# Performance work log

Measured on AMD Instinct MI355X. Metric: run time of the kernel, lower is better.

## Reference

```python
import jax, jax.numpy as jnp
import numpy as np

N, E, F_IN, H, D, HID, G = 50000, 800000, 64, 4, 32, 128, 1024
NEG_SLOPE = 0.2


def setup_inputs():
    key = jax.random.key(0)
    ks = jax.random.split(key, 32)
    inp = {
        "x": jax.random.normal(ks[0], (N, F_IN), dtype=jnp.float32),
        "edge_index": jax.random.randint(ks[1], (2, E), 0, N, dtype=jnp.int64),
        "batch": jnp.sort(jax.random.randint(ks[2], (N,), 0, G, dtype=jnp.int64)),
    }
    dims = [F_IN, HID, HID]
    i = 3
    for l, din in enumerate(dims):
        s = 1.0 / np.sqrt(din)
        inp[f"Wl{l}"] = jax.random.normal(ks[i], (din, H * D), dtype=jnp.float32) * s; i += 1
        inp[f"bl{l}"] = jnp.zeros((H * D,), dtype=jnp.float32)
        inp[f"Wr{l}"] = jax.random.normal(ks[i], (din, H * D), dtype=jnp.float32) * s; i += 1
        inp[f"br{l}"] = jnp.zeros((H * D,), dtype=jnp.float32)
        inp[f"att{l}"] = jax.random.normal(ks[i], (H, D), dtype=jnp.float32) * (1.0 / np.sqrt(D)); i += 1
        inp[f"b{l}"] = jnp.zeros((H * D,), dtype=jnp.float32)
    inp["Wh"] = jax.random.normal(ks[i], (HID, 1), dtype=jnp.float32) * (1.0 / np.sqrt(HID))
    inp["bh"] = jnp.zeros((1,), dtype=jnp.float32)
    return inp


def gatv2_layer(x, src, dst, Wl, bl, Wr, br, att, b):
    # GATv2Conv (eval mode, no dropout): e_ij = att . leaky_relu(Wl x_j + Wr x_i)
    xl = (x @ Wl + bl).reshape(-1, H, D)   # source transform
    xr = (x @ Wr + br).reshape(-1, H, D)   # target transform
    m = xl[src] + xr[dst]                  # [E,H,D]
    e = jnp.where(m >= 0, m, NEG_SLOPE * m)
    score = jnp.einsum("ehd,hd->eh", e, att)          # [E,H]
    smax = jax.ops.segment_max(score, dst, num_segments=N)  # [N,H]
    expv = jnp.exp(score - smax[dst])
    denom = jax.ops.segment_sum(expv, dst, num_segments=N)
    alpha = expv / denom[dst]                          # softmax over in-edges of dst
    agg = jax.ops.segment_sum(alpha[:, :, None] * xl[src], dst, num_segments=N)
    return agg.reshape(-1, H * D) + b


def reference(x, edge_index, batch, Wl0, bl0, Wr0, br0, att0, b0,
              Wl1, bl1, Wr1, br1, att1, b1,
              Wl2, bl2, Wr2, br2, att2, b2, Wh, bh):
    src, dst = edge_index[0], edge_index[1]
    params = [(Wl0, bl0, Wr0, br0, att0, b0),
              (Wl1, bl1, Wr1, br1, att1, b1),
              (Wl2, bl2, Wr2, br2, att2, b2)]
    h = x
    for p in params:
        h = gatv2_layer(h, src, dst, *p)
        h = jax.nn.elu(h)  # dropout inactive in eval
    # global mean pool over graphs
    sums = jax.ops.segment_sum(h, batch, num_segments=G)
    cnt = jax.ops.segment_sum(jnp.ones((h.shape[0],), h.dtype), batch, num_segments=G)
    pooled = sums / jnp.maximum(cnt, 1.0)[:, None]
    return pooled @ Wh + bh
```

## Files before the change

### kernel.cpp

```cpp
#include <hip/hip_runtime.h>
#include <math.h>

#define N_NODES 50000
#define N_EDGES 800000
#define HD 128
#define GG 1024
#define NEG_SLOPE 0.2f
#define SCAN_B 1024
#define NB ((N_NODES + SCAN_B - 1) / SCAN_B)
#define LOG2E 1.4426950408889634f

#if __has_builtin(__builtin_amdgcn_exp2f)
#define EXP2F(x) __builtin_amdgcn_exp2f(x)
#else
#define EXP2F(x) exp2f(x)
#endif

typedef __attribute__((ext_vector_type(8))) short bf16x8;
typedef __attribute__((ext_vector_type(4))) float f32x4;

__device__ __forceinline__ unsigned short f2bf(float v) {
    unsigned u = __float_as_uint(v);
    u += 0x7fff + ((u >> 16) & 1);
    return (unsigned short)(u >> 16);
}
__device__ __forceinline__ float bf2f(unsigned short s) {
    return __uint_as_float((unsigned)s << 16);
}

__global__ void convert_x(const float* __restrict__ x, unsigned short* __restrict__ Xh,
                          unsigned short* __restrict__ Xl, int total)
{
    int i = blockIdx.x * 256 + threadIdx.x;
    if (i >= total) return;
    float v = x[i];
    unsigned short hi = f2bf(v);
    unsigned short lo = f2bf(v - bf2f(hi));
    Xh[i] = hi; Xl[i] = lo;
}

__global__ void convert_w_all(const float* __restrict__ W0l, const float* __restrict__ W0r,
                              const float* __restrict__ W1l, const float* __restrict__ W1r,
                              const float* __restrict__ W2l, const float* __restrict__ W2r,
                              unsigned short* __restrict__ Wth, unsigned short* __restrict__ Wtl)
{
    const int t = blockIdx.x * 256 + threadIdx.x;
    const float* Wl; const float* Wr;
    int c, k, o;
    if (t < 16384) {
        c = t >> 6; k = t & 63; o = t;
        Wl = W0l; Wr = W0r;
    } else if (t < 49152) {
        const int b = t - 16384; c = b >> 7; k = b & 127; o = 32768 + b;
        Wl = W1l; Wr = W1r;
    } else if (t < 81920) {
        const int b = t - 49152; c = b >> 7; k = b & 127; o = 65536 + b;
        Wl = W2l; Wr = W2r;
    } else return;
    const float v = (c < 128) ? Wl[(size_t)k * 128 + c] : Wr[(size_t)k * 128 + (c - 128)];
    const unsigned short hi = f2bf(v);
    Wth[o] = hi;
    Wtl[o] = f2bf(v - bf2f(hi));
}

template<int K>
__launch_bounds__(256)
__global__ void gemm_reg(const unsigned short* __restrict__ Xh, const unsigned short* __restrict__ Xl,
                         const unsigned short* __restrict__ Wth, const unsigned short* __restrict__ Wtl,
                         const float* __restrict__ bl, const float* __restrict__ br,
                         float* __restrict__ Cl, float* __restrict__ Cr, int n)
{
    constexpr int NCH = K / 32;
    constexpr int RT  = (N_NODES + 63) / 64;
    const int tid  = threadIdx.x;
    const int wave = tid >> 6;
    const int lane = tid & 63;
    const int quad = lane >> 4;
    const int l15  = lane & 15;
    const int wid  = blockIdx.x * 4 + wave;
    const int colid = wid & 7;
    const int cb32  = colid * 32;
    const int rs    = wid >> 3;
    const int NS    = (gridDim.x * 4) >> 3;

    bf16x8 Bh[NCH][2], Bo[NCH][2];
    #pragma unroll
    for (int ch = 0; ch < NCH; ch++)
        #pragma unroll
        for (int nt = 0; nt < 2; nt++) {
            const size_t wo = (size_t)(cb32 + nt * 16 + l15) * K + ch * 32 + quad * 8;
            Bh[ch][nt] = *(const bf16x8*)(Wth + wo);
            Bo[ch][nt] = *(const bf16x8*)(Wtl + wo);
        }

    const int cb = cb32 & 127;
    const float* bias = (colid < 4) ? bl : br;
    float* C = (colid < 4) ? Cl : Cr;
    float bv[2];
    bv[0] = bias[cb + l15];
    bv[1] = bias[cb + 16 + l15];

    for (int rt = rs; rt < RT; rt += NS) {
        const int row0 = rt * 64;
        f32x4 acc[4][2];
        #pragma unroll
        for (int mt = 0; mt < 4; mt++) {
            acc[mt][0] = (f32x4){0.f, 0.f, 0.f, 0.f};
            acc[mt][1] = (f32x4){0.f, 0.f, 0.f, 0.f};
        }
        #pragma unroll
        for (int ch = 0; ch < NCH; ch++) {
            bf16x8 ah[4], al[4];
            #pragma unroll
            for (int mt = 0; mt < 4; mt++) {
                int r = row0 + mt * 16 + l15;
                r = (r < n) ? r : (n - 1);
                const size_t go = (size_t)r * K + ch * 32 + quad * 8;
                ah[mt] = *(const bf16x8*)(Xh + go);
                al[mt] = *(const bf16x8*)(Xl + go);
            }
            #pragma unroll
            for (int nt = 0; nt < 2; nt++)
                #pragma unroll
                for (int mt = 0; mt < 4; mt++) {
                    acc[mt][nt] = __builtin_amdgcn_mfma_f32_16x16x32_bf16(ah[mt], Bh[ch][nt], acc[mt][nt], 0, 0, 0);
                    acc[mt][nt] = __builtin_amdgcn_mfma_f32_16x16x32_bf16(ah[mt], Bo[ch][nt], acc[mt][nt], 0, 0, 0);
                    acc[mt][nt] = __builtin_amdgcn_mfma_f32_16x16x32_bf16(al[mt], Bh[ch][nt], acc[mt][nt], 0, 0, 0);
                }
        }
        #pragma unroll
        for (int nt = 0; nt < 2; nt++)
            #pragma unroll
            for (int mt = 0; mt < 4; mt++)
                #pragma unroll
                for (int r = 0; r < 4; r++) {
                    const int row = row0 + mt * 16 + quad * 4 + r;
                    if (row < n)
                        C[(size_t)row * 128 + cb + nt * 16 + l15] = acc[mt][nt][r] + bv[nt];
                }
    }
}

__global__ void deg_hist(const int* __restrict__ dst, int* __restrict__ deg) {
    int e = blockIdx.x * 256 + threadIdx.x;
    if (e < N_EDGES) atomicAdd(&deg[dst[e]], 1);
}

__launch_bounds__(SCAN_B)
__global__ void scan_block(const int* __restrict__ deg, int* __restrict__ rowptr,
                           int* __restrict__ btot)
{
    __shared__ int s[SCAN_B];
    const int tid = threadIdx.x;
    const int i = blockIdx.x * SCAN_B + tid;
    int v = (i < N_NODES) ? deg[i] : 0;
    s[tid] = v;
    __syncthreads();
    for (int off = 1; off < SCAN_B; off <<= 1) {
        int t = (tid >= off) ? s[tid - off] : 0;
        __syncthreads();
        s[tid] += t;
        __syncthreads();
    }
    if (i < N_NODES) rowptr[i] = s[tid] - v;
    if (tid == SCAN_B - 1) btot[blockIdx.x] = s[SCAN_B - 1];
}

__launch_bounds__(256)
__global__ void scan_add(const int* __restrict__ btot, int* __restrict__ rowptr,
                         int* __restrict__ cursor)
{
    __shared__ int sb[NB + 1];
    const int tid = threadIdx.x;
    if (tid < 64) {
        const int v = (tid < NB) ? btot[tid] : 0;
        int incl = v;
        #pragma unroll
        for (int off = 1; off < 64; off <<= 1) {
            const int t = __shfl_up(incl, off);
            if (tid >= off) incl += t;
        }
        if (tid < NB) sb[tid] = incl - v;
        if (tid == NB - 1) sb[NB] = incl;
    }
    __syncthreads();
    const int i = blockIdx.x * 256 + tid;
    if (i < N_NODES) {
        const int r = rowptr[i] + sb[i >> 10];
        rowptr[i] = r;
        cursor[i] = r;
    }
    if (i == N_NODES) rowptr[N_NODES] = sb[NB];
}

__global__ void scatter_csr(const int* __restrict__ src, const int* __restrict__ dst,
                            int* __restrict__ cursor, int* __restrict__ csr_src)
{
    int e = blockIdx.x * 256 + threadIdx.x;
    if (e >= N_EDGES) return;
    int pos = atomicAdd(&cursor[dst[e]], 1);
    csr_src[pos] = src[e];
}

__global__ void build_gptr(const int* __restrict__ batch, int* __restrict__ gptr) {
    int i = blockIdx.x * 256 + threadIdx.x;
    if (i > N_NODES) return;
    if (i == 0) {
        for (int g = 0; g <= batch[0]; g++) gptr[g] = 0;
    } else if (i == N_NODES) {
        for (int g = batch[N_NODES - 1] + 1; g <= GG; g++) gptr[g] = N_NODES;
    } else {
        int b0 = batch[i - 1], b1 = batch[i];
        for (int g = b0 + 1; g <= b1; g++) gptr[g] = i;
    }
}

__launch_bounds__(256)
__global__ void node_attn(const float* __restrict__ xl, const float* __restrict__ xr,
                          const int* __restrict__ rowptr, const int* __restrict__ csr_src,
                          const float* __restrict__ att, const float* __restrict__ bvec,
                          unsigned short* __restrict__ Hh, unsigned short* __restrict__ Hl)
{
    const int node = (blockIdx.x * 256 + threadIdx.x) >> 6;
    const int lane = threadIdx.x & 63;
    if (node >= N_NODES) return;
    const int grp = lane >> 4;
    const int li  = lane & 15;

    const size_t nb = (size_t)node * HD + li * 8;
    const float4 xr0 = *(const float4*)(xr + nb);
    const float4 xr1 = *(const float4*)(xr + nb + 4);
    float4 aw0 = *(const float4*)(att + li * 8);
    float4 aw1 = *(const float4*)(att + li * 8 + 4);
    aw0.x *= LOG2E; aw0.y *= LOG2E; aw0.z *= LOG2E; aw0.w *= LOG2E;
    aw1.x *= LOG2E; aw1.y *= LOG2E; aw1.z *= LOG2E; aw1.w *= LOG2E;
    const int beg = rowptr[node];
    const int end = rowptr[node + 1];

    float m = -1e30f, l = 0.f;
    float4 a0 = make_float4(0.f, 0.f, 0.f, 0.f);
    float4 a1 = make_float4(0.f, 0.f, 0.f, 0.f);

    int e0 = beg + grp;
    int s0 = (e0 < end) ? csr_src[e0] : 0;
    float4 v0 = *(const float4*)(xl + (size_t)s0 * HD + li * 8);
    float4 v1 = *(const float4*)(xl + (size_t)s0 * HD + li * 8 + 4);

    for (int base = beg; base < end; base += 4) {
        const bool valid = (base + grp) < end;
        float4 n0 = v0, n1 = v1;
        if (base + 4 < end) {
            const int e2 = base + 4 + grp;
            const int s2 = (e2 < end) ? csr_src[e2] : 0;
            n0 = *(const float4*)(xl + (size_t)s2 * HD + li * 8);
            n1 = *(const float4*)(xl + (size_t)s2 * HD + li * 8 + 4);
        }
        float t, p;
        t = v0.x + xr0.x; t = fmaxf(t, NEG_SLOPE * t); p  = t * aw0.x;
        t = v0.y + xr0.y; t = fmaxf(t, NEG_SLOPE * t); p  = fmaf(t, aw0.y, p);
        t = v0.z + xr0.z; t = fmaxf(t, NEG_SLOPE * t); p  = fmaf(t, aw0.z, p);
        t = v0.w + xr0.w; t = fmaxf(t, NEG_SLOPE * t); p  = fmaf(t, aw0.w, p);
        t = v1.x + xr1.x; t = fmaxf(t, NEG_SLOPE * t); p  = fmaf(t, aw1.x, p);
        t = v1.y + xr1.y; t = fmaxf(t, NEG_SLOPE * t); p  = fmaf(t, aw1.y, p);
        t = v1.z + xr1.z; t = fmaxf(t, NEG_SLOPE * t); p  = fmaf(t, aw1.z, p);
        t = v1.w + xr1.w; t = fmaxf(t, NEG_SLOPE * t); p  = fmaf(t, aw1.w, p);
        p += __shfl_xor(p, 1);
        p += __shfl_xor(p, 2);

        const bool grow = valid && (p > m + 8.f);
        if (__any(grow)) {
            const float mn = valid ? fmaxf(m, p) : m;
            const float sc = EXP2F(m - mn);
            const float w  = valid ? EXP2F(p - mn) : 0.f;
            l = fmaf(l, sc, w);
            a0.x = fmaf(a0.x, sc, w * v0.x);
            a0.y = fmaf(a0.y, sc, w * v0.y);
            a0.z = fmaf(a0.z, sc, w * v0.z);
            a0.w = fmaf(a0.w, sc, w * v0.w);
            a1.x = fmaf(a1.x, sc, w * v1.x);
            a1.y = fmaf(a1.y, sc, w * v1.y);
            a1.z = fmaf(a1.z, sc, w * v1.z);
            a1.w = fmaf(a1.w, sc, w * v1.w);
            m = mn;
        } else {
            const float w = valid ? EXP2F(p - m) : 0.f;
            l += w;
            a0.x = fmaf(w, v0.x, a0.x);
            a0.y = fmaf(w, v0.y, a0.y);
            a0.z = fmaf(w, v0.z, a0.z);
            a0.w = fmaf(w, v0.w, a0.w);
            a1.x = fmaf(w, v1.x, a1.x);
            a1.y = fmaf(w, v1.y, a1.y);
            a1.z = fmaf(w, v1.z, a1.z);
            a1.w = fmaf(w, v1.w, a1.w);
        }
        v0 = n0; v1 = n1;
    }

    #pragma unroll
    for (int off = 16; off < 64; off <<= 1) {
        const float mo = __shfl_xor(m, off);
        const float lo = __shfl_xor(l, off);
        float4 b0, b1;
        b0.x = __shfl_xor(a0.x, off); b0.y = __shfl_xor(a0.y, off);
        b0.z = __shfl_xor(a0.z, off); b0.w = __shfl_xor(a0.w, off);
        b1.x = __shfl_xor(a1.x, off); b1.y = __shfl_xor(a1.y, off);
        b1.z = __shfl_xor(a1.z, off); b1.w = __shfl_xor(a1.w, off);
        const float mm = fmaxf(m, mo);
        const float e1 = EXP2F(m - mm);
        const float e2 = EXP2F(mo - mm);
        l = l * e1 + lo * e2;
        a0.x = a0.x * e1 + b0.x * e2;
        a0.y = a0.y * e1 + b0.y * e2;
        a0.z = a0.z * e1 + b0.z * e2;
        a0.w = a0.w * e1 + b0.w * e2;
        a1.x = a1.x * e1 + b1.x * e2;
        a1.y = a1.y * e1 + b1.y * e2;
        a1.z = a1.z * e1 + b1.z * e2;
        a1.w = a1.w * e1 + b1.w * e2;
        m = mm;
    }

    if (grp == 0) {
        const float inv = (l > 0.f) ? 1.f / l : 0.f;
        const float4 bb0 = *(const float4*)(bvec + li * 8);
        const float4 bb1 = *(const float4*)(bvec + li * 8 + 4);
        float o[8];
        o[0] = fmaf(a0.x, inv, bb0.x);
        o[1] = fmaf(a0.y, inv, bb0.y);
        o[2] = fmaf(a0.z, inv, bb0.z);
        o[3] = fmaf(a0.w, inv, bb0.w);
        o[4] = fmaf(a1.x, inv, bb1.x);
        o[5] = fmaf(a1.y, inv, bb1.y);
        o[6] = fmaf(a1.z, inv, bb1.z);
        o[7] = fmaf(a1.w, inv, bb1.w);
        bf16x8 hv, lv;
        #pragma unroll
        for (int j = 0; j < 8; j++) {
            float e = (o[j] > 0.f) ? o[j] : expm1f(o[j]);
            unsigned short h = f2bf(e);
            hv[j] = (short)h;
            lv[j] = (short)f2bf(e - bf2f(h));
        }
        *(bf16x8*)(Hh + nb) = hv;
        *(bf16x8*)(Hl + nb) = lv;
    }
}

__launch_bounds__(256)
__global__ void pool_head(const unsigned short* __restrict__ Hh, const unsigned short* __restrict__ Hl,
                          const int* __restrict__ gptr, const float* __restrict__ Wh,
                          const float* __restrict__ bh, float* __restrict__ out)
{
    const int g = (blockIdx.x * 256 + threadIdx.x) >> 6;
    const int lane = threadIdx.x & 63;
    if (g >= GG) return;
    const int b0 = gptr[g], b1 = gptr[g + 1];
    const float2 w = *(const float2*)(Wh + lane * 2);
    float sx = 0.f, sy = 0.f;
    for (int i = b0; i < b1; i++) {
        const unsigned vh = *(const unsigned*)(Hh + (size_t)i * HD + lane * 2);
        const unsigned vl = *(const unsigned*)(Hl + (size_t)i * HD + lane * 2);
        sx += bf2f((unsigned short)(vh & 0xffff)) + bf2f((unsigned short)(vl & 0xffff));
        sy += bf2f((unsigned short)(vh >> 16))    + bf2f((unsigned short)(vl >> 16));
    }
    float d = sx * w.x + sy * w.y;
    d += __shfl_xor(d, 1);
    d += __shfl_xor(d, 2);
    d += __shfl_xor(d, 4);
    d += __shfl_xor(d, 8);
    d += __shfl_xor(d, 16);
    d += __shfl_xor(d, 32);
    if (lane == 0) out[g] = d / fmaxf((float)(b1 - b0), 1.f) + bh[0];
}

extern "C" void kernel_launch(void* const* d_in, const int* in_sizes, int n_in,
                              void* d_out, int out_size, void* d_ws, size_t ws_size,
                              hipStream_t stream)
{
    const float* x     = (const float*)d_in[0];
    const int*   edge  = (const int*)d_in[1];
    const int*   batch = (const int*)d_in[2];
    const int*   src   = edge;
    const int*   dst   = edge + N_EDGES;
    const float* Wh    = (const float*)d_in[21];
    const float* bh    = (const float*)d_in[22];
    float* out = (float*)d_out;

    const size_t N128 = (size_t)N_NODES * HD;
    float* buf_xl = (float*)d_ws;
    float* buf_xr = buf_xl + N128;
    unsigned short* Xh  = (unsigned short*)(buf_xr + N128);
    unsigned short* Xl_ = Xh + N128;
    unsigned short* Wth = Xl_ + N128;
    unsigned short* Wtl = Wth + 3 * 256 * 128;
    int* deg     = (int*)(Wtl + 3 * 256 * 128);
    int* rowptr  = deg + N_NODES;
    int* cursor  = rowptr + N_NODES + 1;
    int* csr_src = cursor + N_NODES;
    int* btot    = csr_src + N_EDGES;
    int* boff    = btot + NB;
    int* gptr    = boff + NB + 1;

    hipMemsetAsync(deg, 0, (size_t)N_NODES * sizeof(int), stream);
    deg_hist<<<(N_EDGES + 255) / 256, 256, 0, stream>>>(dst, deg);
    scan_block<<<NB, SCAN_B, 0, stream>>>(deg, rowptr, btot);
    scan_add<<<(N_NODES + 256) / 256, 256, 0, stream>>>(btot, rowptr, cursor);
    scatter_csr<<<(N_EDGES + 255) / 256, 256, 0, stream>>>(src, dst, cursor, csr_src);
    build_gptr<<<(N_NODES + 256) / 256, 256, 0, stream>>>(batch, gptr);

    convert_x<<<(N_NODES * 64 + 255) / 256, 256, 0, stream>>>(x, Xh, Xl_, N_NODES * 64);
    convert_w_all<<<320, 256, 0, stream>>>(
        (const float*)d_in[3], (const float*)d_in[5],
        (const float*)d_in[9], (const float*)d_in[11],
        (const float*)d_in[15], (const float*)d_in[17],
        Wth, Wtl);

    const int gemm_grid = 768;
    const int attn_grid = (N_NODES + 3) / 4;

    for (int l = 0; l < 3; l++) {
        const float* bl  = (const float*)d_in[4 + 6 * l];
        const float* br  = (const float*)d_in[6 + 6 * l];
        const float* att = (const float*)d_in[7 + 6 * l];
        const float* bb  = (const float*)d_in[8 + 6 * l];

        if (l == 0)
            gemm_reg<64><<<gemm_grid, 256, 0, stream>>>(Xh, Xl_, Wth, Wtl,
                                                        bl, br, buf_xl, buf_xr, N_NODES);
        else
            gemm_reg<128><<<gemm_grid, 256, 0, stream>>>(Xh, Xl_,
                                                         Wth + l * 256 * 128, Wtl + l * 256 * 128,
                                                         bl, br, buf_xl, buf_xr, N_NODES);
        node_attn<<<attn_grid, 256, 0, stream>>>(buf_xl, buf_xr, rowptr, csr_src,
                                                 att, bb, Xh, Xl_);
    }

    pool_head<<<GG / 4, 256, 0, stream>>>(Xh, Xl_, gptr, Wh, bh, out);
}
```

Baseline: 514.2 us.

## Fuse final-layer pooling and head projection into attention kernel via atomics

The last attention layer now computes each node's dot product with the head weights directly and atomically adds it into a per-graph sum, so the final hidden states are never written. A small kernel then divides by node count and adds the bias, replacing the separate pooling kernel. The online-softmax loop also drops its lazy-rescale branch in favour of an always-rescale update using __expf, and splits the score dot product into two accumulators. This saves the last layer's hidden-state writes and the pooling reads, but adds float atomics with nondeterministic summation order and extra exponentials per edge.

```diff
diff --git a/kernel.cpp b/kernel.cpp
--- a/kernel.cpp
+++ b/kernel.cpp
@@ -8,13 +8,6 @@
 #define NEG_SLOPE 0.2f
 #define SCAN_B 1024
 #define NB ((N_NODES + SCAN_B - 1) / SCAN_B)
-#define LOG2E 1.4426950408889634f
-
-#if __has_builtin(__builtin_amdgcn_exp2f)
-#define EXP2F(x) __builtin_amdgcn_exp2f(x)
-#else
-#define EXP2F(x) exp2f(x)
-#endif
 
 typedef __attribute__((ext_vector_type(8))) short bf16x8;
 typedef __attribute__((ext_vector_type(4))) float f32x4;
@@ -215,11 +208,14 @@
     }
 }
 
+template<int LAST>
 __launch_bounds__(256)
 __global__ void node_attn(const float* __restrict__ xl, const float* __restrict__ xr,
                           const int* __restrict__ rowptr, const int* __restrict__ csr_src,
                           const float* __restrict__ att, const float* __restrict__ bvec,
-                          unsigned short* __restrict__ Hh, unsigned short* __restrict__ Hl)
+                          unsigned short* __restrict__ Hh, unsigned short* __restrict__ Hl,
+                          const float* __restrict__ Wh, const int* __restrict__ batch,
+                          float* __restrict__ gsum)
 {
     const int node = (blockIdx.x * 256 + threadIdx.x) >> 6;
     const int lane = threadIdx.x & 63;
@@ -230,10 +226,8 @@
     const size_t nb = (size_t)node * HD + li * 8;
     const float4 xr0 = *(const float4*)(xr + nb);
     const float4 xr1 = *(const float4*)(xr + nb + 4);
-    float4 aw0 = *(const float4*)(att + li * 8);
-    float4 aw1 = *(const float4*)(att + li * 8 + 4);
-    aw0.x *= LOG2E; aw0.y *= LOG2E; aw0.z *= LOG2E; aw0.w *= LOG2E;
-    aw1.x *= LOG2E; aw1.y *= LOG2E; aw1.z *= LOG2E; aw1.w *= LOG2E;
+    const float4 aw0 = *(const float4*)(att + li * 8);
+    const float4 aw1 = *(const float4*)(att + li * 8 + 4);
     const int beg = rowptr[node];
     const int end = rowptr[node + 1];
 
@@ -255,45 +249,32 @@
             n0 = *(const float4*)(xl + (size_t)s2 * HD + li * 8);
             n1 = *(const float4*)(xl + (size_t)s2 * HD + li * 8 + 4);
         }
-        float t, p;
-        t = v0.x + xr0.x; t = fmaxf(t, NEG_SLOPE * t); p  = t * aw0.x;
-        t = v0.y + xr0.y; t = fmaxf(t, NEG_SLOPE * t); p  = fmaf(t, aw0.y, p);
-        t = v0.z + xr0.z; t = fmaxf(t, NEG_SLOPE * t); p  = fmaf(t, aw0.z, p);
-        t = v0.w + xr0.w; t = fmaxf(t, NEG_SLOPE * t); p  = fmaf(t, aw0.w, p);
-        t = v1.x + xr1.x; t = fmaxf(t, NEG_SLOPE * t); p  = fmaf(t, aw1.x, p);
-        t = v1.y + xr1.y; t = fmaxf(t, NEG_SLOPE * t); p  = fmaf(t, aw1.y, p);
-        t = v1.z + xr1.z; t = fmaxf(t, NEG_SLOPE * t); p  = fmaf(t, aw1.z, p);
-        t = v1.w + xr1.w; t = fmaxf(t, NEG_SLOPE * t); p  = fmaf(t, aw1.w, p);
+        float t, pa, pb;
+        t = v0.x + xr0.x; t = fmaxf(t, NEG_SLOPE * t); pa = t * aw0.x;
+        t = v0.y + xr0.y; t = fmaxf(t, NEG_SLOPE * t); pb = t * aw0.y;
+        t = v0.z + xr0.z; t = fmaxf(t, NEG_SLOPE * t); pa = fmaf(t, aw0.z, pa);
+        t = v0.w + xr0.w; t = fmaxf(t, NEG_SLOPE * t); pb = fmaf(t, aw0.w, pb);
+        t = v1.x + xr1.x; t = fmaxf(t, NEG_SLOPE * t); pa = fmaf(t, aw1.x, pa);
+        t = v1.y + xr1.y; t = fmaxf(t, NEG_SLOPE * t); pb = fmaf(t, aw1.y, pb);
+        t = v1.z + xr1.z; t = fmaxf(t, NEG_SLOPE * t); pa = fmaf(t, aw1.z, pa);
+        t = v1.w + xr1.w; t = fmaxf(t, NEG_SLOPE * t); pb = fmaf(t, aw1.w, pb);
+        float p = pa + pb;
         p += __shfl_xor(p, 1);
         p += __shfl_xor(p, 2);
 
-        const bool grow = valid && (p > m + 8.f);
-        if (__any(grow)) {
-            const float mn = valid ? fmaxf(m, p) : m;
-            const float sc = EXP2F(m - mn);
-            const float w  = valid ? EXP2F(p - mn) : 0.f;
-            l = fmaf(l, sc, w);
-            a0.x = fmaf(a0.x, sc, w * v0.x);
-            a0.y = fmaf(a0.y, sc, w * v0.y);
-            a0.z = fmaf(a0.z, sc, w * v0.z);
-            a0.w = fmaf(a0.w, sc, w * v0.w);
-            a1.x = fmaf(a1.x, sc, w * v1.x);
-            a1.y = fmaf(a1.y, sc, w * v1.y);
-            a1.z = fmaf(a1.z, sc, w * v1.z);
-            a1.w = fmaf(a1.w, sc, w * v1.w);
-            m = mn;
-        } else {
-            const float w = valid ? EXP2F(p - m) : 0.f;
-            l += w;
-            a0.x = fmaf(w, v0.x, a0.x);
-            a0.y = fmaf(w, v0.y, a0.y);
-            a0.z = fmaf(w, v0.z, a0.z);
-            a0.w = fmaf(w, v0.w, a0.w);
-            a1.x = fmaf(w, v1.x, a1.x);
-            a1.y = fmaf(w, v1.y, a1.y);
-            a1.z = fmaf(w, v1.z, a1.z);
-            a1.w = fmaf(w, v1.w, a1.w);
-        }
+        const float mn = valid ? fmaxf(m, p) : m;
+        const float w  = valid ? __expf(p - mn) : 0.f;
+        const float sc = __expf(m - mn);
+        l = fmaf(l, sc, w);
+        a0.x = fmaf(a0.x, sc, w * v0.x);
+        a0.y = fmaf(a0.y, sc, w * v0.y);
+        a0.z = fmaf(a0.z, sc, w * v0.z);
+        a0.w = fmaf(a0.w, sc, w * v0.w);
+        a1.x = fmaf(a1.x, sc, w * v1.x);
+        a1.y = fmaf(a1.y, sc, w * v1.y);
+        a1.z = fmaf(a1.z, sc, w * v1.z);
+        a1.w = fmaf(a1.w, sc, w * v1.w);
+        m = mn;
         v0 = n0; v1 = n1;
     }
 
@@ -307,8 +288,8 @@
         b1.x = __shfl_xor(a1.x, off); b1.y = __shfl_xor(a1.y, off);
         b1.z = __shfl_xor(a1.z, off); b1.w = __shfl_xor(a1.w, off);
         const float mm = fmaxf(m, mo);
-        const float e1 = EXP2F(m - mm);
-        const float e2 = EXP2F(mo - mm);
+        const float e1 = __expf(m - mm);
+        const float e2 = __expf(mo - mm);
         l = l * e1 + lo * e2;
         a0.x = a0.x * e1 + b0.x * e2;
         a0.y = a0.y * e1 + b0.y * e2;
@@ -334,44 +315,43 @@
         o[5] = fmaf(a1.y, inv, bb1.y);
         o[6] = fmaf(a1.z, inv, bb1.z);
         o[7] = fmaf(a1.w, inv, bb1.w);
-        bf16x8 hv, lv;
-        #pragma unroll
-        for (int j = 0; j < 8; j++) {
-            float e = (o[j] > 0.f) ? o[j] : expm1f(o[j]);
-            unsigned short h = f2bf(e);
-            hv[j] = (short)h;
-            lv[j] = (short)f2bf(e - bf2f(h));
-        }
-        *(bf16x8*)(Hh + nb) = hv;
-        *(bf16x8*)(Hl + nb) = lv;
-    }
-}
-
-__launch_bounds__(256)
-__global__ void pool_head(const unsigned short* __restrict__ Hh, const unsigned short* __restrict__ Hl,
-                          const int* __restrict__ gptr, const float* __restrict__ Wh,
-                          const float* __restrict__ bh, float* __restrict__ out)
-{
-    const int g = (blockIdx.x * 256 + threadIdx.x) >> 6;
-    const int lane = threadIdx.x & 63;
+        #pragma unroll
+        for (int j = 0; j < 8; j++)
+            o[j] = (o[j] > 0.f) ? o[j] : expm1f(o[j]);
+        if (LAST) {
+            const float4 w0 = *(const float4*)(Wh + li * 8);
+            const float4 w1 = *(const float4*)(Wh + li * 8 + 4);
+            float da = o[0] * w0.x + o[2] * w0.z;
+            float db = o[1] * w0.y + o[3] * w0.w;
+            da = fmaf(o[4], w1.x, da); db = fmaf(o[5], w1.y, db);
+            da = fmaf(o[6], w1.z, da); db = fmaf(o[7], w1.w, db);
+            float d = da + db;
+            d += __shfl_xor(d, 1);
+            d += __shfl_xor(d, 2);
+            d += __shfl_xor(d, 4);
+            d += __shfl_xor(d, 8);
+            if (li == 0) atomicAdd(&gsum[batch[node]], d);
+        } else {
+            bf16x8 hv, lv;
+            #pragma unroll
+            for (int j = 0; j < 8; j++) {
+                unsigned short h = f2bf(o[j]);
+                hv[j] = (short)h;
+                lv[j] = (short)f2bf(o[j] - bf2f(h));
+            }
+            *(bf16x8*)(Hh + nb) = hv;
+            *(bf16x8*)(Hl + nb) = lv;
+        }
+    }
+}
+
+__global__ void finish_head(const float* __restrict__ gsum, const int* __restrict__ gptr,
+                            const float* __restrict__ bh, float* __restrict__ out)
+{
+    const int g = blockIdx.x * 256 + threadIdx.x;
     if (g >= GG) return;
-    const int b0 = gptr[g], b1 = gptr[g + 1];
-    const float2 w = *(const float2*)(Wh + lane * 2);
-    float sx = 0.f, sy = 0.f;
-    for (int i = b0; i < b1; i++) {
-        const unsigned vh = *(const unsigned*)(Hh + (size_t)i * HD + lane * 2);
-        const unsigned vl = *(const unsigned*)(Hl + (size_t)i * HD + lane * 2);
-        sx += bf2f((unsigned short)(vh & 0xffff)) + bf2f((unsigned short)(vl & 0xffff));
-        sy += bf2f((unsigned short)(vh >> 16))    + bf2f((unsigned short)(vl >> 16));
-    }
-    float d = sx * w.x + sy * w.y;
-    d += __shfl_xor(d, 1);
-    d += __shfl_xor(d, 2);
-    d += __shfl_xor(d, 4);
-    d += __shfl_xor(d, 8);
-    d += __shfl_xor(d, 16);
-    d += __shfl_xor(d, 32);
-    if (lane == 0) out[g] = d / fmaxf((float)(b1 - b0), 1.f) + bh[0];
+    const int cnt = gptr[g + 1] - gptr[g];
+    out[g] = gsum[g] / fmaxf((float)cnt, 1.f) + bh[0];
 }
 
 extern "C" void kernel_launch(void* const* d_in, const int* in_sizes, int n_in,
@@ -395,14 +375,14 @@
     unsigned short* Wth = Xl_ + N128;
     unsigned short* Wtl = Wth + 3 * 256 * 128;
     int* deg     = (int*)(Wtl + 3 * 256 * 128);
-    int* rowptr  = deg + N_NODES;
+    float* gsum  = (float*)(deg + N_NODES);
+    int* rowptr  = (int*)(gsum + GG);
     int* cursor  = rowptr + N_NODES + 1;
     int* csr_src = cursor + N_NODES;
     int* btot    = csr_src + N_EDGES;
-    int* boff    = btot + NB;
-    int* gptr    = boff + NB + 1;
-
-    hipMemsetAsync(deg, 0, (size_t)N_NODES * sizeof(int), stream);
+    int* gptr    = btot + NB;
+
+    hipMemsetAsync(deg, 0, (size_t)(N_NODES + GG) * sizeof(int), stream);
     deg_hist<<<(N_EDGES + 255) / 256, 256, 0, stream>>>(dst, deg);
     scan_block<<<NB, SCAN_B, 0, stream>>>(deg, rowptr, btot);
     scan_add<<<(N_NODES + 256) / 256, 256, 0, stream>>>(btot, rowptr, cursor);
@@ -432,9 +412,15 @@
             gemm_reg<128><<<gemm_grid, 256, 0, stream>>>(Xh, Xl_,
                                                          Wth + l * 256 * 128, Wtl + l * 256 * 128,
                                                          bl, br, buf_xl, buf_xr, N_NODES);
-        node_attn<<<attn_grid, 256, 0, stream>>>(buf_xl, buf_xr, rowptr, csr_src,
-                                                 att, bb, Xh, Xl_);
-    }
-
-    pool_head<<<GG / 4, 256, 0, stream>>>(Xh, Xl_, gptr, Wh, bh, out);
-}
+        if (l < 2)
+            node_attn<0><<<attn_grid, 256, 0, stream>>>(buf_xl, buf_xr, rowptr, csr_src,
+                                                        att, bb, Xh, Xl_,
+                                                        nullptr, nullptr, nullptr);
+        else
+            node_attn<1><<<attn_grid, 256, 0, stream>>>(buf_xl, buf_xr, rowptr, csr_src,
+                                                        att, bb, nullptr, nullptr,
+                                                        Wh, batch, gsum);
+    }
+
+    finish_head<<<GG / 256, 256, 0, stream>>>(gsum, gptr, bh, out);
+}
```

Measured after the change: 543.9 us. 5.8% more time.
